# Kernel optimization log

Hardware: AMD Instinct MI355X
Metric: run time of the kernel (lower is better)

Reference implementation:

```python
import jax, jax.numpy as jnp
import numpy as np

B, T, I, H, O = 8192, 128, 28, 200, 10


def setup_inputs() -> dict:
    key = jax.random.key(0)
    ks = jax.random.split(key, 7)
    s_ih = 1.0 / np.sqrt(H)
    return {
        "x": jax.random.normal(ks[0], (B, T, I), dtype=jnp.float32),
        "W_ih": jax.random.uniform(ks[1], (H, I), jnp.float32, -s_ih, s_ih),
        "W_hh": jax.random.uniform(ks[2], (H, H), jnp.float32, -s_ih, s_ih),
        "b_ih": jax.random.uniform(ks[3], (H,), jnp.float32, -s_ih, s_ih),
        "b_hh": jax.random.uniform(ks[4], (H,), jnp.float32, -s_ih, s_ih),
        "W_fc": jax.random.uniform(ks[5], (O, H), jnp.float32, -s_ih, s_ih),
        "b_fc": jax.random.uniform(ks[6], (O,), jnp.float32, -s_ih, s_ih),
    }


def reference(x, W_ih, W_hh, b_ih, b_hh, W_fc, b_fc):
    # Precompute input projections for all timesteps in one GEMM: [B,T,H]
    xp = jnp.einsum("bti,hi->bth", x, W_ih) + b_ih + b_hh
    h0 = jnp.zeros((x.shape[0], W_hh.shape[0]), dtype=x.dtype)

    def step(h, xp_t):
        # h_t = relu(x_t W_ih^T + b_ih + h_{t-1} W_hh^T + b_hh)
        h = jax.nn.relu(xp_t + h @ W_hh.T)
        return h, None

    # scan over time: xp transposed to [T,B,H]
    h_last, _ = jax.lax.scan(step, h0, jnp.swapaxes(xp, 0, 1))
    # out[:, -1, :] then fc1
    return h_last @ W_fc.T + b_fc
```

## Files before the change

### kernel.cpp

```cpp
#include <hip/hip_runtime.h>

typedef float f4v __attribute__((ext_vector_type(4)));
typedef float f2v __attribute__((ext_vector_type(2)));
typedef short s8v __attribute__((ext_vector_type(8)));

#define TT 128
#define II 28
#define HH 200
#define BB 16
#define NT 256
#define SH 232
#define KX 224
#define CH 8
#define XW (CH * BB * II)

__device__ __forceinline__ unsigned pk_hu(float a, float b) {
    unsigned ua = __builtin_bit_cast(unsigned, a) + 0x8000u;
    unsigned ub = __builtin_bit_cast(unsigned, b) + 0x8000u;
    return __builtin_amdgcn_perm(ub, ua, 0x07060302);
}
__device__ __forceinline__ short f2bf(float f) {
    return (short)((__builtin_bit_cast(unsigned, f) + 0x8000u) >> 16);
}

__global__ __launch_bounds__(NT, 2)
void rnn_r7(const float* __restrict__ x,
            const float* __restrict__ W_ih,
            const float* __restrict__ W_hh,
            const float* __restrict__ b_ih,
            const float* __restrict__ b_hh,
            const float* __restrict__ W_fc,
            const float* __restrict__ b_fc,
            float* __restrict__ out)
{
    __shared__ __align__(16) short Hs[2][BB][SH];
    __shared__ __align__(16) float Xl[2][XW + 8];

    const int tid  = threadIdx.x;
    const int lane = tid & 63;
    const int q    = lane >> 4;
    const int lr   = lane & 15;
    const int wave = tid >> 6;
    const int b0   = blockIdx.x * BB;

    const int first = (wave == 0) ? 0 : 1 + 3 * wave;
    const int cnt   = (wave == 0) ? 4 : 3;

    for (int i = tid; i < 2 * BB * SH / 2; i += NT) ((int*)Hs)[i] = 0;

    s8v Af[4][8];
    #pragma unroll
    for (int u = 0; u < 4; ++u) {
        const int j = 16 * (first + u) + lr;
        #pragma unroll
        for (int kc = 0; kc < 8; ++kc) {
            union { short s[8]; s8v v; } tv;
            #pragma unroll
            for (int i = 0; i < 8; ++i) {
                const int k = 32 * kc + 8 * q + i;
                float w = 0.0f;
                if (u < cnt && j < HH) {
                    if (k < HH)                    w = W_hh[j * HH + k];
                    else if (k >= KX && k < KX+II) w = W_ih[j * II + (k - KX)];
                }
                tv.s[i] = f2bf(w);
            }
            Af[u][kc] = tv.v;
        }
    }

    f4v biasv[4];
    #pragma unroll
    for (int u = 0; u < 4; ++u) {
        f4v bv = {0.f, 0.f, 0.f, 0.f};
        #pragma unroll
        for (int i = 0; i < 4; ++i) {
            const int j = 16 * (first + u) + 4 * q + i;
            if (u < cnt && j < HH) bv[i] = b_ih[j] + b_hh[j];
        }
        biasv[u] = bv;
    }

    const int wv = wave - 2;
    long xoff[7];
    #pragma unroll
    for (int e = 0; e < 7; ++e) {
        if (wv >= 0) {
            const int m  = ((wv * 7 + e) << 6) + lane;
            const int tl = m / 112;
            const int rm = m - tl * 112;
            const int r  = rm / 7;
            const int c4 = rm - r * 7;
            xoff[e] = ((long)(b0 + r) * TT + tl) * II + c4 * 4;
        } else xoff[e] = 0;
    }
    auto load_chunk = [&](int cc) {
        if (wv >= 0) {
            float* dbase = &Xl[cc & 1][(wv * 7) * 256];
            #pragma unroll
            for (int e = 0; e < 7; ++e) {
                const float* src = x + xoff[e] + (long)cc * (CH * II);
                __builtin_amdgcn_global_load_lds(
                    (const __attribute__((address_space(1))) void*)src,
                    (__attribute__((address_space(3))) void*)(dbase + e * 256),
                    16, 0, 0);
            }
        }
    };

    load_chunk(0);
    __syncthreads();

    for (int c = 0; c < TT / CH; ++c) {
        if (c + 1 < TT / CH) load_chunk(c + 1);
        #pragma unroll
        for (int s = 0; s < CH; ++s) {
            const int t  = c * CH + s;
            const int pb = t & 1;

            s8v bf[7];
            #pragma unroll
            for (int kc = 0; kc < 7; ++kc)
                bf[kc] = *(const s8v*)&Hs[pb][lr][32 * kc + 8 * q];

            const float* xr = &Xl[c & 1][s * (BB * II) + lr * II + 8 * q];
            const f2v x0 = *(const f2v*)(xr + 0);
            const f2v x1 = *(const f2v*)(xr + 2);
            const f2v x2 = *(const f2v*)(xr + 4);
            const f2v x3 = *(const f2v*)(xr + 6);
            union { unsigned u4[4]; s8v v; } xf;
            xf.u4[0] = pk_hu(x0.x, x0.y);
            xf.u4[1] = pk_hu(x1.x, x1.y);
            xf.u4[2] = pk_hu(x2.x, x2.y);
            xf.u4[3] = pk_hu(x3.x, x3.y);

            f4v acc[4];
            #pragma unroll
            for (int u = 0; u < 4; ++u)
                if (u < cnt)
                    acc[u] = __builtin_amdgcn_mfma_f32_16x16x32_bf16(Af[u][7], xf.v, biasv[u], 0, 0, 0);
            #pragma unroll
            for (int kc = 0; kc < 7; ++kc) {
                #pragma unroll
                for (int u = 0; u < 4; ++u)
                    if (u < cnt)
                        acc[u] = __builtin_amdgcn_mfma_f32_16x16x32_bf16(Af[u][kc], bf[kc], acc[u], 0, 0, 0);
            }

            #pragma unroll
            for (int u = 0; u < 4; ++u) {
                if (u < cnt) {
                    const int jt = first + u;
                    const float r0 = fmaxf(acc[u].x, 0.f), r1 = fmaxf(acc[u].y, 0.f);
                    const float r2 = fmaxf(acc[u].z, 0.f), r3 = fmaxf(acc[u].w, 0.f);
                    int2 hv;
                    hv.x = (int)pk_hu(r0, r1);
                    hv.y = (int)pk_hu(r2, r3);
                    *(int2*)&Hs[pb ^ 1][lr][16 * jt + 4 * q] = hv;
                }
            }
            __syncthreads();
        }
    }

    if (tid < BB * 10) {
        const int o = tid >> 4, r = tid & 15;
        float sacc = b_fc[o];
        for (int k = 0; k < HH; ++k) {
            const float hk = __builtin_bit_cast(float,
                (unsigned)((unsigned short)Hs[0][r][k]) << 16);
            sacc = fmaf(hk, W_fc[o * HH + k], sacc);
        }
        __builtin_nontemporal_store(sacc, &out[(long)(b0 + r) * 10 + o]);
    }
}

extern "C" void kernel_launch(void* const* d_in, const int* in_sizes, int n_in,
                              void* d_out, int out_size, void* d_ws, size_t ws_size,
                              hipStream_t stream) {
    const float* x    = (const float*)d_in[0];
    const float* W_ih = (const float*)d_in[1];
    const float* W_hh = (const float*)d_in[2];
    const float* b_ih = (const float*)d_in[3];
    const float* b_hh = (const float*)d_in[4];
    const float* W_fc = (const float*)d_in[5];
    const float* b_fc = (const float*)d_in[6];
    float* out = (float*)d_out;

    rnn_r7<<<dim3(8192 / BB), dim3(NT), 0, stream>>>(
        x, W_ih, W_hh, b_ih, b_hh, W_fc, b_fc, out);
}
```

Baseline: 300.5 us.

## Split hidden tiles over eight waves, fold bias into MFMA, prepack x to bf16

Doubles the block to 512 threads so each wave owns at most two hidden tiles instead of three or four, which shortens the serial MFMA chain per timestep. The bias is folded into the input-projection MFMA through extra K columns: a hi/lo bf16 split of the bias multiplied by a constant 1.0 column in the packed x buffer. Once per 8-step chunk, x is converted to bf16 in LDS and then reused by all waves, replacing per-step float loads and packing. Per-step barriers become a raw lgkmcnt wait plus s_barrier, MFMA sections get raised priority, and h loads are interleaved with the MFMAs. The cost is two block-wide barriers per chunk around a single-buffered x staging area, and higher occupancy demands on registers and LDS.

```diff
diff --git a/kernel.cpp b/kernel.cpp
--- a/kernel.cpp
+++ b/kernel.cpp
@@ -1,18 +1,20 @@
 #include <hip/hip_runtime.h>
 
 typedef float f4v __attribute__((ext_vector_type(4)));
-typedef float f2v __attribute__((ext_vector_type(2)));
 typedef short s8v __attribute__((ext_vector_type(8)));
 
 #define TT 128
 #define II 28
 #define HH 200
 #define BB 16
-#define NT 256
+#define NT 512
 #define SH 232
+#define XS 40
+#define CH 8
 #define KX 224
-#define CH 8
-#define XW (CH * BB * II)
+#define NCH (TT / CH)
+
+template <bool B> struct BC { static constexpr bool value = B; };
 
 __device__ __forceinline__ unsigned pk_hu(float a, float b) {
     unsigned ua = __builtin_bit_cast(unsigned, a) + 0x8000u;
@@ -22,9 +24,14 @@
 __device__ __forceinline__ short f2bf(float f) {
     return (short)((__builtin_bit_cast(unsigned, f) + 0x8000u) >> 16);
 }
-
-__global__ __launch_bounds__(NT, 2)
-void rnn_r7(const float* __restrict__ x,
+__device__ __forceinline__ float bf2f(short s) {
+    return __builtin_bit_cast(float, ((unsigned)(unsigned short)s) << 16);
+}
+
+#define STEP_BAR() asm volatile("s_waitcnt lgkmcnt(0)\n\ts_barrier" ::: "memory")
+
+__global__ __launch_bounds__(NT, 4)
+void rnn_r9(const float* __restrict__ x,
             const float* __restrict__ W_ih,
             const float* __restrict__ W_hh,
             const float* __restrict__ b_ih,
@@ -34,24 +41,52 @@
             float* __restrict__ out)
 {
     __shared__ __align__(16) short Hs[2][BB][SH];
-    __shared__ __align__(16) float Xl[2][XW + 8];
+    __shared__ __align__(16) short Xb[CH][BB][XS];
+    __shared__ __align__(16) float Xl[CH * BB * II];
 
     const int tid  = threadIdx.x;
     const int lane = tid & 63;
     const int q    = lane >> 4;
     const int lr   = lane & 15;
-    const int wave = tid >> 6;
+    const int wave = __builtin_amdgcn_readfirstlane(tid >> 6);
     const int b0   = blockIdx.x * BB;
 
-    const int first = (wave == 0) ? 0 : 1 + 3 * wave;
-    const int cnt   = (wave == 0) ? 4 : 3;
-
-    for (int i = tid; i < 2 * BB * SH / 2; i += NT) ((int*)Hs)[i] = 0;
-
-    s8v Af[4][8];
+    const bool two = (wave < 5);
+    const int jt0  = two ? 2 * wave : 10 + (wave - 5);
+    const int jt1  = two ? 2 * wave + 1 : 13;
+
+    const int nIss = (wave < 6) ? 2 : 1;
+    const int e0   = (wave < 6) ? 2 * wave : 12 + (wave - 6);
+    unsigned xoff[2];
     #pragma unroll
-    for (int u = 0; u < 4; ++u) {
-        const int j = 16 * (first + u) + lr;
+    for (int k = 0; k < 2; ++k) {
+        const int e  = e0 + k;
+        const int m  = (e << 6) + lane;
+        const int tl = m / 112;
+        const int rm = m - tl * 112;
+        const int r  = rm / 7;
+        const int c4 = rm - r * 7;
+        xoff[k] = (unsigned)(((((b0 + r) * TT + tl) * II) + c4 * 4) * 4);
+    }
+    auto issue_dma = [&](int c) {
+        #pragma unroll
+        for (int k = 0; k < 2; ++k) {
+            if (k < nIss) {
+                const char* src = (const char*)x + (xoff[k] + (unsigned)c * (CH * II * 4));
+                float* dst = &Xl[(e0 + k) * 256];
+                __builtin_amdgcn_global_load_lds(
+                    (const __attribute__((address_space(1))) void*)src,
+                    (__attribute__((address_space(3))) void*)dst, 16, 0, 0);
+            }
+        }
+    };
+
+    issue_dma(0);
+
+    s8v Af[2][8];
+    #pragma unroll
+    for (int u = 0; u < 2; ++u) {
+        const int j = 16 * (u ? jt1 : jt0) + lr;
         #pragma unroll
         for (int kc = 0; kc < 8; ++kc) {
             union { short s[8]; s8v v; } tv;
@@ -59,9 +94,15 @@
             for (int i = 0; i < 8; ++i) {
                 const int k = 32 * kc + 8 * q + i;
                 float w = 0.0f;
-                if (u < cnt && j < HH) {
-                    if (k < HH)                    w = W_hh[j * HH + k];
-                    else if (k >= KX && k < KX+II) w = W_ih[j * II + (k - KX)];
+                if (j < HH) {
+                    if (k < HH)                     w = W_hh[j * HH + k];
+                    else if (k >= KX && k < KX+II)  w = W_ih[j * II + (k - KX)];
+                    else if (k == KX + II) {
+                        w = b_ih[j] + b_hh[j];
+                    } else if (k == KX + II + 1) {
+                        const float bs = b_ih[j] + b_hh[j];
+                        w = bs - bf2f(f2bf(bs));
+                    }
                 }
                 tv.s[i] = f2bf(w);
             }
@@ -69,109 +110,105 @@
         }
     }
 
-    f4v biasv[4];
-    #pragma unroll
-    for (int u = 0; u < 4; ++u) {
-        f4v bv = {0.f, 0.f, 0.f, 0.f};
-        #pragma unroll
-        for (int i = 0; i < 4; ++i) {
-            const int j = 16 * (first + u) + 4 * q + i;
-            if (u < cnt && j < HH) bv[i] = b_ih[j] + b_hh[j];
-        }
-        biasv[u] = bv;
-    }
-
-    const int wv = wave - 2;
-    long xoff[7];
-    #pragma unroll
-    for (int e = 0; e < 7; ++e) {
-        if (wv >= 0) {
-            const int m  = ((wv * 7 + e) << 6) + lane;
-            const int tl = m / 112;
-            const int rm = m - tl * 112;
-            const int r  = rm / 7;
-            const int c4 = rm - r * 7;
-            xoff[e] = ((long)(b0 + r) * TT + tl) * II + c4 * 4;
-        } else xoff[e] = 0;
-    }
-    auto load_chunk = [&](int cc) {
-        if (wv >= 0) {
-            float* dbase = &Xl[cc & 1][(wv * 7) * 256];
-            #pragma unroll
-            for (int e = 0; e < 7; ++e) {
-                const float* src = x + xoff[e] + (long)cc * (CH * II);
-                __builtin_amdgcn_global_load_lds(
-                    (const __attribute__((address_space(1))) void*)src,
-                    (__attribute__((address_space(3))) void*)(dbase + e * 256),
-                    16, 0, 0);
-            }
-        }
-    };
-
-    load_chunk(0);
-    __syncthreads();
-
-    for (int c = 0; c < TT / CH; ++c) {
-        if (c + 1 < TT / CH) load_chunk(c + 1);
+    for (int i = tid; i < (2 * BB * SH) / 2; i += NT) ((int*)Hs)[i] = 0;
+    for (int i = tid; i < (CH * BB * XS) / 2; i += NT)
+        ((int*)Xb)[i] = (i % 20 == 14) ? 0x3f803f80 : 0;
+
+    const f4v Z = {0.f, 0.f, 0.f, 0.f};
+
+    auto steps = [&](auto TWOC) {
+        constexpr bool TWO = decltype(TWOC)::value;
         #pragma unroll
         for (int s = 0; s < CH; ++s) {
-            const int t  = c * CH + s;
-            const int pb = t & 1;
-
-            s8v bf[7];
+            const int pb = s & 1;
+            const short* hrow = &Hs[pb][lr][8 * q];
+            s8v g0 = *(const s8v*)(hrow);
+            s8v g1 = *(const s8v*)(hrow + 32);
+            s8v g2 = *(const s8v*)(hrow + 64);
+            s8v g3 = *(const s8v*)(hrow + 96);
+            const s8v xb = *(const s8v*)&Xb[s][lr][8 * q];
+            __builtin_amdgcn_s_setprio(1);
+            f4v a0 = __builtin_amdgcn_mfma_f32_16x16x32_bf16(Af[0][7], xb, Z, 0, 0, 0);
+            f4v a1;
+            if constexpr (TWO) a1 = __builtin_amdgcn_mfma_f32_16x16x32_bf16(Af[1][7], xb, Z, 0, 0, 0);
+            a0 = __builtin_amdgcn_mfma_f32_16x16x32_bf16(Af[0][0], g0, a0, 0, 0, 0);
+            if constexpr (TWO) a1 = __builtin_amdgcn_mfma_f32_16x16x32_bf16(Af[1][0], g0, a1, 0, 0, 0);
+            g0 = *(const s8v*)(hrow + 128);
+            a0 = __builtin_amdgcn_mfma_f32_16x16x32_bf16(Af[0][1], g1, a0, 0, 0, 0);
+            if constexpr (TWO) a1 = __builtin_amdgcn_mfma_f32_16x16x32_bf16(Af[1][1], g1, a1, 0, 0, 0);
+            g1 = *(const s8v*)(hrow + 160);
+            a0 = __builtin_amdgcn_mfma_f32_16x16x32_bf16(Af[0][2], g2, a0, 0, 0, 0);
+            if constexpr (TWO) a1 = __builtin_amdgcn_mfma_f32_16x16x32_bf16(Af[1][2], g2, a1, 0, 0, 0);
+            g2 = *(const s8v*)(hrow + 192);
+            a0 = __builtin_amdgcn_mfma_f32_16x16x32_bf16(Af[0][3], g3, a0, 0, 0, 0);
+            if constexpr (TWO) a1 = __builtin_amdgcn_mfma_f32_16x16x32_bf16(Af[1][3], g3, a1, 0, 0, 0);
+            a0 = __builtin_amdgcn_mfma_f32_16x16x32_bf16(Af[0][4], g0, a0, 0, 0, 0);
+            if constexpr (TWO) a1 = __builtin_amdgcn_mfma_f32_16x16x32_bf16(Af[1][4], g0, a1, 0, 0, 0);
+            a0 = __builtin_amdgcn_mfma_f32_16x16x32_bf16(Af[0][5], g1, a0, 0, 0, 0);
+            if constexpr (TWO) a1 = __builtin_amdgcn_mfma_f32_16x16x32_bf16(Af[1][5], g1, a1, 0, 0, 0);
+            a0 = __builtin_amdgcn_mfma_f32_16x16x32_bf16(Af[0][6], g2, a0, 0, 0, 0);
+            if constexpr (TWO) a1 = __builtin_amdgcn_mfma_f32_16x16x32_bf16(Af[1][6], g2, a1, 0, 0, 0);
+            __builtin_amdgcn_s_setprio(0);
+            {
+                const int wb = pb ^ 1;
+                int2 hv;
+                hv.x = (int)pk_hu(fmaxf(a0.x, 0.f), fmaxf(a0.y, 0.f));
+                hv.y = (int)pk_hu(fmaxf(a0.z, 0.f), fmaxf(a0.w, 0.f));
+                *(int2*)&Hs[wb][lr][16 * jt0 + 4 * q] = hv;
+                if constexpr (TWO) {
+                    hv.x = (int)pk_hu(fmaxf(a1.x, 0.f), fmaxf(a1.y, 0.f));
+                    hv.y = (int)pk_hu(fmaxf(a1.z, 0.f), fmaxf(a1.w, 0.f));
+                    *(int2*)&Hs[wb][lr][16 * jt1 + 4 * q] = hv;
+                }
+            }
+            if (s < CH - 1) STEP_BAR();
+        }
+    };
+
+    #pragma unroll 1
+    for (int c = 0; c < NCH; ++c) {
+        __syncthreads();
+        if (tid < 448) {
+            const f4v v0 = *(const f4v*)&Xl[tid * 8];
+            const f4v v1 = *(const f4v*)&Xl[tid * 8 + 4];
+            const unsigned d[4] = { pk_hu(v0.x, v0.y), pk_hu(v0.z, v0.w),
+                                    pk_hu(v1.x, v1.y), pk_hu(v1.z, v1.w) };
             #pragma unroll
-            for (int kc = 0; kc < 7; ++kc)
-                bf[kc] = *(const s8v*)&Hs[pb][lr][32 * kc + 8 * q];
-
-            const float* xr = &Xl[c & 1][s * (BB * II) + lr * II + 8 * q];
-            const f2v x0 = *(const f2v*)(xr + 0);
-            const f2v x1 = *(const f2v*)(xr + 2);
-            const f2v x2 = *(const f2v*)(xr + 4);
-            const f2v x3 = *(const f2v*)(xr + 6);
-            union { unsigned u4[4]; s8v v; } xf;
-            xf.u4[0] = pk_hu(x0.x, x0.y);
-            xf.u4[1] = pk_hu(x1.x, x1.y);
-            xf.u4[2] = pk_hu(x2.x, x2.y);
-            xf.u4[3] = pk_hu(x3.x, x3.y);
-
-            f4v acc[4];
-            #pragma unroll
-            for (int u = 0; u < 4; ++u)
-                if (u < cnt)
-                    acc[u] = __builtin_amdgcn_mfma_f32_16x16x32_bf16(Af[u][7], xf.v, biasv[u], 0, 0, 0);
-            #pragma unroll
-            for (int kc = 0; kc < 7; ++kc) {
-                #pragma unroll
-                for (int u = 0; u < 4; ++u)
-                    if (u < cnt)
-                        acc[u] = __builtin_amdgcn_mfma_f32_16x16x32_bf16(Af[u][kc], bf[kc], acc[u], 0, 0, 0);
-            }
-
-            #pragma unroll
-            for (int u = 0; u < 4; ++u) {
-                if (u < cnt) {
-                    const int jt = first + u;
-                    const float r0 = fmaxf(acc[u].x, 0.f), r1 = fmaxf(acc[u].y, 0.f);
-                    const float r2 = fmaxf(acc[u].z, 0.f), r3 = fmaxf(acc[u].w, 0.f);
-                    int2 hv;
-                    hv.x = (int)pk_hu(r0, r1);
-                    hv.y = (int)pk_hu(r2, r3);
-                    *(int2*)&Hs[pb ^ 1][lr][16 * jt + 4 * q] = hv;
-                }
-            }
-            __syncthreads();
-        }
-    }
-
+            for (int dk = 0; dk < 4; ++dk) {
+                const int kk = tid * 4 + dk;
+                const int t  = kk / 224;
+                const int k2 = kk - t * 224;
+                const int r  = k2 / 14;
+                const int cp = k2 - r * 14;
+                ((int*)Xb)[t * 320 + r * 20 + cp] = (int)d[dk];
+            }
+        }
+        STEP_BAR();
+        if (c + 1 < NCH) issue_dma(c + 1);
+        if (two) steps(BC<true>{});
+        else     steps(BC<false>{});
+    }
+
+    __syncthreads();
     if (tid < BB * 10) {
         const int o = tid >> 4, r = tid & 15;
-        float sacc = b_fc[o];
-        for (int k = 0; k < HH; ++k) {
-            const float hk = __builtin_bit_cast(float,
-                (unsigned)((unsigned short)Hs[0][r][k]) << 16);
-            sacc = fmaf(hk, W_fc[o * HH + k], sacc);
-        }
-        __builtin_nontemporal_store(sacc, &out[(long)(b0 + r) * 10 + o]);
+        const float* wrow = W_fc + o * HH;
+        float acc = b_fc[o];
+        #pragma unroll 1
+        for (int kb = 0; kb < 25; ++kb) {
+            const s8v hv = *(const s8v*)&Hs[0][r][kb * 8];
+            const f4v w0 = *(const f4v*)(wrow + kb * 8);
+            const f4v w1 = *(const f4v*)(wrow + kb * 8 + 4);
+            acc = fmaf(bf2f(hv[0]), w0.x, acc);
+            acc = fmaf(bf2f(hv[1]), w0.y, acc);
+            acc = fmaf(bf2f(hv[2]), w0.z, acc);
+            acc = fmaf(bf2f(hv[3]), w0.w, acc);
+            acc = fmaf(bf2f(hv[4]), w1.x, acc);
+            acc = fmaf(bf2f(hv[5]), w1.y, acc);
+            acc = fmaf(bf2f(hv[6]), w1.z, acc);
+            acc = fmaf(bf2f(hv[7]), w1.w, acc);
+        }
+        __builtin_nontemporal_store(acc, &out[(long)(b0 + r) * 10 + o]);
     }
 }
 
@@ -187,6 +224,6 @@
     const float* b_fc = (const float*)d_in[6];
     float* out = (float*)d_out;
 
-    rnn_r7<<<dim3(8192 / BB), dim3(NT), 0, stream>>>(
+    rnn_r9<<<dim3(8192 / BB), dim3(NT), 0, stream>>>(
         x, W_ih, W_hh, b_ih, b_hh, W_fc, b_fc, out);
 }
```

Result: faster. 289.3 us (-3.8%).
